# Kernel tuning notes

Measured on AMD Instinct MI355X. Metric: run time of the kernel, lower is better.

Reference implementation:

```python
import jax, jax.numpy as jnp
import numpy as np

N = 262144  # points per batch (~4096 rays x 64 samples)
FDIM = 64   # plane feature dim
S = 512     # base plane resolution


def setup_inputs() -> dict:
    key = jax.random.key(0)
    ks = jax.random.split(key, 10)
    x = jax.random.uniform(ks[0], (N, 3), dtype=jnp.float32, minval=-1.0, maxval=1.0)
    rays_o = jnp.array([[0.0, 0.0, 1.5]], dtype=jnp.float32)  # ray origin; distances straddle 1.5/2.0
    scale = jnp.ones((3,), dtype=jnp.float32)
    plane = lambda k, s: jax.random.normal(k, (FDIM, s, s), dtype=jnp.float32)
    return {
        'x': x, 'rays_o': rays_o, 'scale': scale,
        'xy_plane': plane(ks[1], S), 'yz_plane': plane(ks[2], S), 'xz_plane': plane(ks[3], S),
        'xy_plane1': plane(ks[4], S // 2), 'yz_plane1': plane(ks[5], S // 2), 'xz_plane1': plane(ks[6], S // 2),
        'xy_plane2': plane(ks[7], S // 4), 'yz_plane2': plane(ks[8], S // 4), 'xz_plane2': plane(ks[9], S // 4),
    }


def bilinear_sample(plane, coords):
    """F.grid_sample(mode='bilinear', align_corners=True, padding_mode='zeros').
    plane: [C, H, W]; coords: [N, 2] with (x, y) in [-1, 1] (x indexes W).
    Returns [N, C]."""
    C, H, W = plane.shape
    fx = (coords[:, 0] + 1.0) * 0.5 * (W - 1)
    fy = (coords[:, 1] + 1.0) * 0.5 * (H - 1)
    x0 = jnp.floor(fx)
    y0 = jnp.floor(fy)
    wx = fx - x0
    wy = fy - y0
    x0i = x0.astype(jnp.int32)
    y0i = y0.astype(jnp.int32)

    def gather(xi, yi):
        valid = (xi >= 0) & (xi < W) & (yi >= 0) & (yi < H)
        xc = jnp.clip(xi, 0, W - 1)
        yc = jnp.clip(yi, 0, H - 1)
        v = plane[:, yc, xc]  # [C, N]
        return jnp.where(valid[None, :], v, 0.0)

    v00 = gather(x0i, y0i)
    v01 = gather(x0i + 1, y0i)
    v10 = gather(x0i, y0i + 1)
    v11 = gather(x0i + 1, y0i + 1)
    out = (v00 * (1 - wx) * (1 - wy) + v01 * wx * (1 - wy)
           + v10 * (1 - wx) * wy + v11 * wx * wy)  # [C, N]
    return out.T


def forward(x, rays_o, scale, xy0, yz0, xz0, xy1, yz1, xz1, xy2, yz2, xz2):
    xs = x * scale[None, :]
    xy_c = xs[:, :2]                                   # (x, y)
    xz_c = jnp.stack([xs[:, 0], xs[:, 2]], axis=-1)    # (x, z)
    yz_c = xs[:, 1:]                                   # (y, z)

    # laplace breakpoints: first index with distance > 1.5 / > 2.0 from rays_o[0]
    d = jnp.linalg.norm(rays_o[0][None, :] - xs, axis=-1)
    c1 = d > 1.5
    c2 = d > 2.0
    break1 = jnp.where(c1.any(), jnp.argmax(c1), 0)
    break2 = jnp.where(c2.any(), jnp.argmax(c2), 0)
    idx = jnp.arange(x.shape[0])
    # level 0: [0, break1), level 1: [break1, break2), level 2: [break2, N)
    level = jnp.where(idx < break1, 0, jnp.where(idx < break2, 1, 2))[:, None]

    def tri(p0, p1, p2, c):
        s0 = bilinear_sample(p0, c)
        s1 = bilinear_sample(p1, c)
        s2 = bilinear_sample(p2, c)
        # laplace: level1 = fine + half, level2 = fine + half + quarter
        return jnp.where(level == 0, s0, jnp.where(level == 1, s0 + s1, s0 + s1 + s2))

    return (tri(xy0, xy1, xy2, xy_c)
            + tri(xz0, xz1, xz2, xz_c)
            + tri(yz0, yz1, yz2, yz_c))


def reference(x, rays_o, scale, xy_plane, yz_plane, xz_plane, xy_plane1, yz_plane1, xz_plane1, xy_plane2, yz_plane2, xz_plane2):
    return forward(x, rays_o, scale, xy_plane, yz_plane, xz_plane,
                   xy_plane1, yz_plane1, xz_plane1,
                   xy_plane2, yz_plane2, xz_plane2)
```

## Files before the change

kernel.cpp:

```cpp
#include <hip/hip_runtime.h>
#include <hip/hip_fp16.h>

#define NPTS 262144
#define FDIM 64

typedef float vfloat4 __attribute__((ext_vector_type(4)));

__global__ __launch_bounds__(256) void break_kernel(const float* __restrict__ x,
                                                    const float* __restrict__ rays_o,
                                                    const float* __restrict__ scale,
                                                    unsigned* __restrict__ breaks) {
  const unsigned t = blockIdx.x * 256u + threadIdx.x;
  const float r0 = rays_o[0], r1 = rays_o[1], r2 = rays_o[2];
  const float s0 = scale[0], s1 = scale[1], s2 = scale[2];
  unsigned b1 = 0xFFFFFFFFu, b2 = 0xFFFFFFFFu;
  for (unsigned p = t; p < NPTS; p += 65536u) {
    const float dx = r0 - x[p * 3 + 0] * s0;
    const float dy = r1 - x[p * 3 + 1] * s1;
    const float dz = r2 - x[p * 3 + 2] * s2;
    const float d = sqrtf(__fadd_rn(__fadd_rn(__fmul_rn(dx, dx), __fmul_rn(dy, dy)),
                                    __fmul_rn(dz, dz)));
    if (d > 1.5f) b1 = min(b1, p);
    if (d > 2.0f) b2 = min(b2, p);
  }
  __shared__ unsigned sb1[256];
  __shared__ unsigned sb2[256];
  sb1[threadIdx.x] = b1;
  sb2[threadIdx.x] = b2;
  __syncthreads();
  for (int s = 128; s > 0; s >>= 1) {
    if ((int)threadIdx.x < s) {
      sb1[threadIdx.x] = min(sb1[threadIdx.x], sb1[threadIdx.x + s]);
      sb2[threadIdx.x] = min(sb2[threadIdx.x], sb2[threadIdx.x + s]);
    }
    __syncthreads();
  }
  if (threadIdx.x == 0) {
    atomicMin(&breaks[0], sb1[0]);
    atomicMin(&breaks[1], sb2[0]);
  }
}

struct TransposeArgs {
  const float* src[9];
  __half* dst[9];
  int tile_hi[9];
  int SS[9];
};

__global__ __launch_bounds__(256) void transpose_all(TransposeArgs a) {
  __shared__ __half lds[64 * 66];
  const int tile = blockIdx.x;
  int pi = 0;
#pragma unroll
  for (int i = 0; i < 9; ++i) {
    if (tile >= a.tile_hi[i]) pi = i + 1;
  }
  const int lo = (pi == 0) ? 0 : a.tile_hi[pi - 1];
  const float* __restrict__ src = a.src[pi];
  __half* __restrict__ dst = a.dst[pi];
  const size_t SS = (size_t)a.SS[pi];
  const size_t p0 = (size_t)(tile - lo) * 64;

  const int t = threadIdx.x;
  const int px4 = t & 15;
  const int cg = t >> 4;
#pragma unroll
  for (int it = 0; it < 4; ++it) {
    const int c = it * 16 + cg;
    const float4 v = *(const float4*)(src + (size_t)c * SS + p0 + (size_t)px4 * 4);
    lds[(px4 * 4 + 0) * 66 + c] = __float2half(v.x);
    lds[(px4 * 4 + 1) * 66 + c] = __float2half(v.y);
    lds[(px4 * 4 + 2) * 66 + c] = __float2half(v.z);
    lds[(px4 * 4 + 3) * 66 + c] = __float2half(v.w);
  }
  __syncthreads();
  const int c8 = t & 7;
  const int pxo = t >> 3;
#pragma unroll
  for (int it = 0; it < 2; ++it) {
    const int px = it * 32 + pxo;
    const unsigned* w = (const unsigned*)(lds + px * 66 + c8 * 8);
    uint4 v;
    v.x = w[0]; v.y = w[1]; v.z = w[2]; v.w = w[3];
    *(uint4*)(dst + (p0 + (size_t)px) * FDIM + c8 * 8) = v;
  }
}

union H8 { uint4 u; __half h[8]; };

__device__ __forceinline__ void bilinear_weights(int W, float cx, float cy,
                                                 float& w00, float& w01, float& w10, float& w11,
                                                 int& xc0, int& xc1, int& yc0, int& yc1) {
  const float Wm1 = (float)(W - 1);
  const float fx = (cx + 1.0f) * 0.5f * Wm1;
  const float fy = (cy + 1.0f) * 0.5f * Wm1;
  const float x0f = floorf(fx), y0f = floorf(fy);
  const float wx = fx - x0f, wy = fy - y0f;
  const int ix = (int)x0f, iy = (int)y0f;
  const int ix1 = ix + 1, iy1 = iy + 1;
  const bool vx0 = (ix >= 0) && (ix < W);
  const bool vx1 = (ix1 >= 0) && (ix1 < W);
  const bool vy0 = (iy >= 0) && (iy < W);
  const bool vy1 = (iy1 >= 0) && (iy1 < W);
  xc0 = min(max(ix, 0), W - 1);
  xc1 = min(max(ix1, 0), W - 1);
  yc0 = min(max(iy, 0), W - 1);
  yc1 = min(max(iy1, 0), W - 1);
  w00 = (1.0f - wx) * (1.0f - wy) * (float)(vx0 && vy0);
  w01 = wx * (1.0f - wy) * (float)(vx1 && vy0);
  w10 = (1.0f - wx) * wy * (float)(vx0 && vy1);
  w11 = wx * wy * (float)(vx1 && vy1);
}

__device__ __forceinline__ void sample8_t(const __half* __restrict__ pl, int W,
                                          float cx, float cy, int j8, float acc[8]) {
  float w00, w01, w10, w11;
  int xc0, xc1, yc0, yc1;
  bilinear_weights(W, cx, cy, w00, w01, w10, w11, xc0, xc1, yc0, yc1);
  const __half* b00 = pl + ((size_t)(yc0 * W + xc0) * FDIM + j8);
  const __half* b01 = pl + ((size_t)(yc0 * W + xc1) * FDIM + j8);
  const __half* b10 = pl + ((size_t)(yc1 * W + xc0) * FDIM + j8);
  const __half* b11 = pl + ((size_t)(yc1 * W + xc1) * FDIM + j8);
  H8 v00, v01, v10, v11;
  v00.u = *(const uint4*)b00;
  v01.u = *(const uint4*)b01;
  v10.u = *(const uint4*)b10;
  v11.u = *(const uint4*)b11;
#pragma unroll
  for (int k = 0; k < 8; ++k) {
    acc[k] += w00 * __half2float(v00.h[k]) + w01 * __half2float(v01.h[k]) +
              w10 * __half2float(v10.h[k]) + w11 * __half2float(v11.h[k]);
  }
}

__device__ __forceinline__ void sample8_d(const float* __restrict__ pl, int W,
                                          float cx, float cy, int j8, float acc[8]) {
  float w00, w01, w10, w11;
  int xc0, xc1, yc0, yc1;
  bilinear_weights(W, cx, cy, w00, w01, w10, w11, xc0, xc1, yc0, yc1);
  const size_t SS = (size_t)W * W;
  const int i00 = yc0 * W + xc0, i01 = yc0 * W + xc1;
  const int i10 = yc1 * W + xc0, i11 = yc1 * W + xc1;
#pragma unroll
  for (int k = 0; k < 8; ++k) {
    const size_t co = (size_t)(j8 + k) * SS;
    acc[k] += w00 * pl[co + i00] + w01 * pl[co + i01] +
              w10 * pl[co + i10] + w11 * pl[co + i11];
  }
}

struct PlanesH { const __half* p[9]; };
struct PlanesF { const float* p[9]; };

__global__ __launch_bounds__(256) void sample_kernel(const float* __restrict__ x,
                                                     const float* __restrict__ scale,
                                                     const unsigned* __restrict__ breaks,
                                                     PlanesH tp, float* __restrict__ out) {
  const int t = blockIdx.x * 256 + threadIdx.x;
  const int p = t >> 3;
  const int j8 = (t & 7) * 8;
  const float s0 = scale[0], s1 = scale[1], s2 = scale[2];
  const float xs0 = x[p * 3 + 0] * s0;
  const float xs1 = x[p * 3 + 1] * s1;
  const float xs2 = x[p * 3 + 2] * s2;
  unsigned b1 = breaks[0]; if (b1 >= NPTS) b1 = 0;
  unsigned b2 = breaks[1]; if (b2 >= NPTS) b2 = 0;
  const unsigned pu = (unsigned)p;
  const int level = (pu < b1) ? 0 : ((pu < b2) ? 1 : 2);
  float acc[8];
#pragma unroll
  for (int k = 0; k < 8; ++k) acc[k] = 0.0f;
  sample8_t(tp.p[0], 512, xs0, xs1, j8, acc);
  sample8_t(tp.p[1], 512, xs1, xs2, j8, acc);
  sample8_t(tp.p[2], 512, xs0, xs2, j8, acc);
  if (level >= 1) {
    sample8_t(tp.p[3], 256, xs0, xs1, j8, acc);
    sample8_t(tp.p[4], 256, xs1, xs2, j8, acc);
    sample8_t(tp.p[5], 256, xs0, xs2, j8, acc);
  }
  if (level >= 2) {
    sample8_t(tp.p[6], 128, xs0, xs1, j8, acc);
    sample8_t(tp.p[7], 128, xs1, xs2, j8, acc);
    sample8_t(tp.p[8], 128, xs0, xs2, j8, acc);
  }
  float* o = out + (size_t)p * FDIM + j8;
  vfloat4 lo = {acc[0], acc[1], acc[2], acc[3]};
  vfloat4 hi = {acc[4], acc[5], acc[6], acc[7]};
  __builtin_nontemporal_store(lo, (vfloat4*)o);
  __builtin_nontemporal_store(hi, (vfloat4*)(o + 4));
}

__global__ __launch_bounds__(256) void sample_kernel_direct(const float* __restrict__ x,
                                                            const float* __restrict__ scale,
                                                            const unsigned* __restrict__ breaks,
                                                            PlanesF tp, float* __restrict__ out) {
  const int t = blockIdx.x * 256 + threadIdx.x;
  const int p = t >> 3;
  const int j8 = (t & 7) * 8;
  const float s0 = scale[0], s1 = scale[1], s2 = scale[2];
  const float xs0 = x[p * 3 + 0] * s0;
  const float xs1 = x[p * 3 + 1] * s1;
  const float xs2 = x[p * 3 + 2] * s2;
  unsigned b1 = breaks[0]; if (b1 >= NPTS) b1 = 0;
  unsigned b2 = breaks[1]; if (b2 >= NPTS) b2 = 0;
  const unsigned pu = (unsigned)p;
  const int level = (pu < b1) ? 0 : ((pu < b2) ? 1 : 2);
  float acc[8];
#pragma unroll
  for (int k = 0; k < 8; ++k) acc[k] = 0.0f;
  sample8_d(tp.p[0], 512, xs0, xs1, j8, acc);
  sample8_d(tp.p[1], 512, xs1, xs2, j8, acc);
  sample8_d(tp.p[2], 512, xs0, xs2, j8, acc);
  if (level >= 1) {
    sample8_d(tp.p[3], 256, xs0, xs1, j8, acc);
    sample8_d(tp.p[4], 256, xs1, xs2, j8, acc);
    sample8_d(tp.p[5], 256, xs0, xs2, j8, acc);
  }
  if (level >= 2) {
    sample8_d(tp.p[6], 128, xs0, xs1, j8, acc);
    sample8_d(tp.p[7], 128, xs1, xs2, j8, acc);
    sample8_d(tp.p[8], 128, xs0, xs2, j8, acc);
  }
  float4* o4 = (float4*)(out + (size_t)p * FDIM + j8);
  o4[0] = make_float4(acc[0], acc[1], acc[2], acc[3]);
  o4[1] = make_float4(acc[4], acc[5], acc[6], acc[7]);
}

extern "C" void kernel_launch(void* const* d_in, const int* in_sizes, int n_in,
                              void* d_out, int out_size, void* d_ws, size_t ws_size,
                              hipStream_t stream) {
  const float* x = (const float*)d_in[0];
  const float* rays_o = (const float*)d_in[1];
  const float* scale = (const float*)d_in[2];
  const float* pl32[9];
  for (int i = 0; i < 9; ++i) pl32[i] = (const float*)d_in[3 + i];
  float* out = (float*)d_out;

  unsigned char* ws = (unsigned char*)d_ws;
  unsigned* breaks = (unsigned*)ws;

  (void)hipMemsetAsync(d_ws, 0xFF, 8, stream);
  break_kernel<<<256, 256, 0, stream>>>(x, rays_o, scale, breaks);

  const int Ss[3] = {512, 256, 128};
  size_t need = 256;
  for (int l = 0; l < 3; ++l) need += 3 * (size_t)Ss[l] * Ss[l] * FDIM * sizeof(__half);

  if (ws_size >= need) {
    PlanesH tp;
    TransposeArgs ta;
    size_t off = 256;
    int tiles_acc = 0;
    for (int l = 0; l < 3; ++l) {
      const int S = Ss[l];
      const int SS = S * S;
      for (int o = 0; o < 3; ++o) {
        const int i = l * 3 + o;
        __half* dst = (__half*)(ws + off);
        tp.p[i] = dst;
        ta.src[i] = pl32[i];
        ta.dst[i] = dst;
        ta.SS[i] = SS;
        tiles_acc += SS / 64;
        ta.tile_hi[i] = tiles_acc;
        off += (size_t)SS * FDIM * sizeof(__half);
      }
    }
    transpose_all<<<tiles_acc, 256, 0, stream>>>(ta);
    sample_kernel<<<(NPTS * 8) / 256, 256, 0, stream>>>(x, scale, breaks, tp, out);
  } else {
    PlanesF tf;
    for (int i = 0; i < 9; ++i) tf.p[i] = pl32[i];
    sample_kernel_direct<<<(NPTS * 8) / 256, 256, 0, stream>>>(x, scale, breaks, tf, out);
  }
}
```

Measured before the change: 446.2 us.

## Sort points by Morton-ordered spatial cell before plane sampling

Adds a counting sort of points into a 32^3 Morton-ordered grid (histogram, single-block scan, atomic scatter) and has the sample kernel process points in that order. Spatially nearby points then share warps, so their gathers from the transposed half-precision planes hit the same cache lines and reuse L2. The cost is three extra kernel launches, a memset and atomics, plus output writes that become scattered per point (still 32-byte contiguous per thread).

```diff
diff --git a/kernel.cpp b/kernel.cpp
--- a/kernel.cpp
+++ b/kernel.cpp
@@ -3,6 +3,7 @@
 
 #define NPTS 262144
 #define FDIM 64
+#define NCELL 32768
 
 typedef float vfloat4 __attribute__((ext_vector_type(4)));
 
@@ -39,6 +40,62 @@
     atomicMin(&breaks[0], sb1[0]);
     atomicMin(&breaks[1], sb2[0]);
   }
+}
+
+__device__ __forceinline__ unsigned part5(unsigned v) {
+  v &= 31u;
+  v = (v | (v << 8)) & 0x100Fu;
+  v = (v | (v << 4)) & 0x10C3u;
+  v = (v | (v << 2)) & 0x1249u;
+  return v;
+}
+
+__device__ __forceinline__ unsigned cell_key(float x0, float x1, float x2) {
+  const int cx = min(max((int)((x0 + 1.0f) * 16.0f), 0), 31);
+  const int cy = min(max((int)((x1 + 1.0f) * 16.0f), 0), 31);
+  const int cz = min(max((int)((x2 + 1.0f) * 16.0f), 0), 31);
+  return part5((unsigned)cx) | (part5((unsigned)cy) << 1) | (part5((unsigned)cz) << 2);
+}
+
+__global__ __launch_bounds__(256) void hist_kernel(const float* __restrict__ x,
+                                                   const float* __restrict__ scale,
+                                                   unsigned* __restrict__ hist) {
+  const unsigned t = blockIdx.x * 256u + threadIdx.x;
+  const float s0 = scale[0], s1 = scale[1], s2 = scale[2];
+  const unsigned key = cell_key(x[t * 3 + 0] * s0, x[t * 3 + 1] * s1, x[t * 3 + 2] * s2);
+  atomicAdd(&hist[key], 1u);
+}
+
+__global__ __launch_bounds__(256) void scan_kernel(unsigned* __restrict__ hist) {
+  const int tid = threadIdx.x;
+  unsigned s = 0;
+  for (int i = 0; i < 128; ++i) s += hist[tid * 128 + i];
+  __shared__ unsigned ls[256];
+  ls[tid] = s;
+  __syncthreads();
+  for (int d = 1; d < 256; d <<= 1) {
+    const unsigned add = (tid >= d) ? ls[tid - d] : 0u;
+    __syncthreads();
+    ls[tid] += add;
+    __syncthreads();
+  }
+  unsigned run = ls[tid] - s;
+  for (int i = 0; i < 128; ++i) {
+    const unsigned h = hist[tid * 128 + i];
+    hist[tid * 128 + i] = run;
+    run += h;
+  }
+}
+
+__global__ __launch_bounds__(256) void scatter_kernel(const float* __restrict__ x,
+                                                      const float* __restrict__ scale,
+                                                      unsigned* __restrict__ offs,
+                                                      unsigned* __restrict__ order) {
+  const unsigned t = blockIdx.x * 256u + threadIdx.x;
+  const float s0 = scale[0], s1 = scale[1], s2 = scale[2];
+  const unsigned key = cell_key(x[t * 3 + 0] * s0, x[t * 3 + 1] * s1, x[t * 3 + 2] * s2);
+  const unsigned pos = atomicAdd(&offs[key], 1u);
+  order[pos] = t;
 }
 
 struct TransposeArgs {
@@ -156,9 +213,11 @@
 __global__ __launch_bounds__(256) void sample_kernel(const float* __restrict__ x,
                                                      const float* __restrict__ scale,
                                                      const unsigned* __restrict__ breaks,
+                                                     const unsigned* __restrict__ order,
                                                      PlanesH tp, float* __restrict__ out) {
   const int t = blockIdx.x * 256 + threadIdx.x;
-  const int p = t >> 3;
+  const int slot = t >> 3;
+  const int p = (int)order[slot];
   const int j8 = (t & 7) * 8;
   const float s0 = scale[0], s1 = scale[1], s2 = scale[2];
   const float xs0 = x[p * 3 + 0] * s0;
@@ -239,18 +298,26 @@
 
   unsigned char* ws = (unsigned char*)d_ws;
   unsigned* breaks = (unsigned*)ws;
+  unsigned* hist = (unsigned*)(ws + 256);
+  unsigned* order = (unsigned*)(ws + 256 + NCELL * 4);
+  const size_t planes_off = 256 + (size_t)NCELL * 4 + (size_t)NPTS * 4;
 
   (void)hipMemsetAsync(d_ws, 0xFF, 8, stream);
   break_kernel<<<256, 256, 0, stream>>>(x, rays_o, scale, breaks);
 
   const int Ss[3] = {512, 256, 128};
-  size_t need = 256;
+  size_t need = planes_off;
   for (int l = 0; l < 3; ++l) need += 3 * (size_t)Ss[l] * Ss[l] * FDIM * sizeof(__half);
 
   if (ws_size >= need) {
+    (void)hipMemsetAsync(hist, 0, NCELL * 4, stream);
+    hist_kernel<<<NPTS / 256, 256, 0, stream>>>(x, scale, hist);
+    scan_kernel<<<1, 256, 0, stream>>>(hist);
+    scatter_kernel<<<NPTS / 256, 256, 0, stream>>>(x, scale, hist, order);
+
     PlanesH tp;
     TransposeArgs ta;
-    size_t off = 256;
+    size_t off = planes_off;
     int tiles_acc = 0;
     for (int l = 0; l < 3; ++l) {
       const int S = Ss[l];
@@ -268,7 +335,7 @@
       }
     }
     transpose_all<<<tiles_acc, 256, 0, stream>>>(ta);
-    sample_kernel<<<(NPTS * 8) / 256, 256, 0, stream>>>(x, scale, breaks, tp, out);
+    sample_kernel<<<(NPTS * 8) / 256, 256, 0, stream>>>(x, scale, breaks, order, tp, out);
   } else {
     PlanesF tf;
     for (int i = 0; i < 9; ++i) tf.p[i] = pl32[i];
```

After: 437.8 us. No clear change (-1.9%).
